# Kernel tuning notes

Measured on AMD Instinct MI355X. Metric: run time of the kernel, lower is better.

The kernel has to match this reference:

```python
import jax, jax.numpy as jnp
import numpy as np

B, L, H, V = 16, 1024, 512, 32000
HALF = H // 2
ALPHA = 0.95
EPS_NORM = 1e-12
EPS_LN = 1e-5


def setup_inputs() -> dict:
    key = jax.random.key(0)
    ks = jax.random.split(key, 12)
    s = 0.02
    return {
        "seq": jax.random.randint(ks[0], (B, L), 0, V),
        "embed": jax.random.normal(ks[1], (V, H), jnp.float32) * s,
        "ff_w1": jax.random.normal(ks[2], (2 * H, H), jnp.float32) * s,
        "ff_b1": jnp.zeros((2 * H,), jnp.float32),
        "ff_w2": jax.random.normal(ks[3], (H, 2 * H), jnp.float32) * s,
        "ff_b2": jnp.zeros((H,), jnp.float32),
        "gamma": jnp.ones((H,), jnp.float32),
        "beta": jnp.zeros((H,), jnp.float32),
        "sem_w": jax.random.normal(ks[4], (HALF, H), jnp.float32) * s,
        "epi_w": jax.random.normal(ks[5], (HALF, H), jnp.float32) * s,
        "rp_w": jax.random.normal(ks[6], (H, H), jnp.float32) * s,
        "rp_b": jnp.zeros((H,), jnp.float32),
        "out_w": jax.random.normal(ks[7], (V, H), jnp.float32) * s,
        "out_b": jnp.zeros((V,), jnp.float32),
    }


def _layernorm(x, gamma, beta):
    mu = jnp.mean(x, axis=-1, keepdims=True)
    var = jnp.mean(jnp.square(x - mu), axis=-1, keepdims=True)
    return (x - mu) * jax.lax.rsqrt(var + EPS_LN) * gamma + beta


def _l2norm(k):
    # F.normalize: k / max(||k||_2, eps)
    n = jnp.sqrt(jnp.sum(jnp.square(k), axis=-1, keepdims=True))
    return k / jnp.maximum(n, EPS_NORM)


def reference(seq, embed, ff_w1, ff_b1, ff_w2, ff_b2, gamma, beta,
              sem_w, epi_w, rp_w, rp_b, out_w, out_b):
    h = embed[seq]  # [B, L, H]
    ff = jnp.maximum(jnp.einsum('blh,fh->blf', h, ff_w1) + ff_b1, 0.0)
    ff = jnp.einsum('blf,hf->blh', ff, ff_w2) + ff_b2
    h = _layernorm(h + ff, gamma, beta)  # [B, L, H]

    # precompute all keys, time-major for scan: [L, B, half]
    ks_all = jnp.einsum('blh,ch->lbc', h, sem_w)
    ke_all = jnp.einsum('blh,ch->lbc', h, epi_w)

    def step(carry, inp):
        Ms, Me = carry                      # [B, half, half]
        ks, ke = inp                        # [B, half]
        kns = _l2norm(ks)
        kne = _l2norm(ke)
        vps = jnp.einsum('bij,bj->bi', Ms, kns)
        vpe = jnp.einsum('bij,bj->bi', Me, kne)
        Ds = (ks - vps)[:, :, None] * kns[:, None, :]
        De = (ke - vpe)[:, :, None] * kne[:, None, :]
        Ms = Ms + (1.0 - ALPHA) * Ds
        Me = Me + (1.0 - ALPHA) * De
        return (Ms, Me), None

    M0 = jnp.zeros((B, HALF, HALF), h.dtype)
    (M_s, M_e), _ = jax.lax.scan(step, (M0, M0), (ks_all[:L - 1], ke_all[:L - 1]))

    qs = ks_all[L - 1]  # sem_p(h[:, -1])
    qe = ke_all[L - 1]  # epi_p(h[:, -1])
    cs = jnp.einsum('bij,bj->bi', M_s, qs)
    ce = jnp.einsum('bij,bj->bi', M_e, qe)
    c = jnp.concatenate([cs, ce], axis=-1)  # [B, H]
    r = jnp.einsum('bh,gh->bg', c, rp_w) + rp_b
    return jnp.einsum('bh,vh->bv', r, out_w) + out_b  # [B, V]
```

## Files before the change

kernel.cpp:

```cpp
#include <hip/hip_runtime.h>
#include <stdint.h>

#define Bsz 16
#define Lsz 1024
#define Hsz 512
#define Vsz 32000
#define HALF 256
#define BETA 0.05f

typedef unsigned short u16;
typedef __attribute__((ext_vector_type(8))) short short8;
typedef __attribute__((ext_vector_type(4))) float f32x4;

__device__ __forceinline__ float bf2f(u16 u) { return __uint_as_float(((unsigned int)u) << 16); }
__device__ __forceinline__ u16 f2bf(float f) {
    unsigned int u = __float_as_uint(f);
    return (u16)((u + 0x7FFFu + ((u >> 16) & 1u)) >> 16);
}
__device__ __forceinline__ u16 f2h(float f) {
    _Float16 h = (_Float16)f;
    return *(u16*)&h;
}
__device__ __forceinline__ bool mode_f32(const void* gamma) {
    return *(const unsigned int*)gamma == 0x3F800000u;
}

__device__ __forceinline__ float wave_sum(float p) {
    p += __shfl_xor(p, 32, 64);
    p += __shfl_xor(p, 16, 64);
    p += __shfl_xor(p, 8, 64);
    p += __shfl_xor(p, 4, 64);
    p += __shfl_xor(p, 2, 64);
    p += __shfl_xor(p, 1, 64);
    return p;
}

__device__ __forceinline__ void cvt8(const void* src, u16* dst, int i, bool f32m) {
    union { u16 u[8]; uint4 q; } o;
    if (f32m) {
        const float* s = (const float*)src + i;
        const float4 a = *(const float4*)s;
        const float4 b = *(const float4*)(s + 4);
        o.u[0] = f2bf(a.x); o.u[1] = f2bf(a.y); o.u[2] = f2bf(a.z); o.u[3] = f2bf(a.w);
        o.u[4] = f2bf(b.x); o.u[5] = f2bf(b.y); o.u[6] = f2bf(b.z); o.u[7] = f2bf(b.w);
    } else {
        o.q = *(const uint4*)((const u16*)src + i);
    }
    *(uint4*)(dst + i) = o.q;
}

__global__ __launch_bounds__(256)
void cvt_all(const void* s0, const void* s1, const void* s2, const void* s3,
             const void* s4, const void* s5, const void* s6, const void* s7,
             const void* s8, const void* s9, const void* s10,
             u16* d0, u16* d1, u16* d2, u16* d3, u16* d4, u16* d5, u16* d6,
             u16* d7, u16* d8, u16* d9, u16* d10, const void* gamma) {
    const bool f32m = mode_f32(gamma);
    const int g = blockIdx.x * 256 + threadIdx.x;
    const void* src; u16* dst; int off;
    if      (g < 65536)  { src = s0;  dst = d0;  off = g; }
    else if (g < 131072) { src = s1;  dst = d1;  off = g - 65536; }
    else if (g < 147456) { src = s2;  dst = d2;  off = g - 131072; }
    else if (g < 163840) { src = s3;  dst = d3;  off = g - 147456; }
    else if (g < 196608) { src = s4;  dst = d4;  off = g - 163840; }
    else if (g < 196736) { src = s5;  dst = d5;  off = g - 196608; }
    else if (g < 196800) { src = s6;  dst = d6;  off = g - 196736; }
    else if (g < 196864) { src = s7;  dst = d7;  off = g - 196800; }
    else if (g < 196928) { src = s8;  dst = d8;  off = g - 196864; }
    else if (g < 196992) { src = s9;  dst = d9;  off = g - 196928; }
    else if (g < 200992) { src = s10; dst = d10; off = g - 196992; }
    else return;
    cvt8(src, dst, off * 8, f32m);
}

__global__ __launch_bounds__(256)
void gather_kernel(const int* __restrict__ seq, const void* __restrict__ embed,
                   u16* __restrict__ h0, const void* __restrict__ gamma) {
    const bool f32m = mode_f32(gamma);
    const int row = blockIdx.x * 4 + (threadIdx.x >> 6);
    const int lane = threadIdx.x & 63;
    const int tok = seq[row];
    union { u16 u[8]; uint4 q; } o;
    if (f32m) {
        const float* e = (const float*)embed + (size_t)tok * Hsz + lane * 8;
        const float4 a = *(const float4*)e;
        const float4 b = *(const float4*)(e + 4);
        o.u[0] = f2bf(a.x); o.u[1] = f2bf(a.y); o.u[2] = f2bf(a.z); o.u[3] = f2bf(a.w);
        o.u[4] = f2bf(b.x); o.u[5] = f2bf(b.y); o.u[6] = f2bf(b.z); o.u[7] = f2bf(b.w);
    } else {
        o.q = *((const uint4*)((const u16*)embed + (size_t)tok * Hsz) + lane);
    }
    *((uint4*)(h0 + (size_t)row * Hsz) + lane) = o.q;
}

template <int EPI>
__global__ __launch_bounds__(256)
void gemm128(const u16* __restrict__ A, const u16* __restrict__ B0,
             const u16* __restrict__ B1, const u16* __restrict__ bias,
             const u16* resid, void* Cout, u16* __restrict__ kT,
             int M, int N, int K) {
    __shared__ u16 Als[128 * 32];
    __shared__ u16 Bls[128 * 32];
    const int tid = threadIdx.x;
    const int wave = tid >> 6, lane = tid & 63;
    const int m0 = blockIdx.y * 128, n0 = blockIdx.x * 128;

    const u16* Bt;
    if (EPI == 2) Bt = (n0 < HALF) ? (B0 + (size_t)n0 * K) : (B1 + (size_t)(n0 - HALF) * K);
    else          Bt = B0 + (size_t)n0 * K;
    const u16* At = A + (size_t)m0 * K;

    const int wm = wave >> 1, wn = wave & 1;
    const int srow = lane >> 2;
    const int sk = (lane & 3) * 8;
    const int fr = lane & 15;
    const int fq = (lane >> 4) * 8;

    f32x4 acc[4][4];
#pragma unroll
    for (int i = 0; i < 4; i++)
#pragma unroll
        for (int j = 0; j < 4; j++) acc[i][j] = (f32x4){0.f, 0.f, 0.f, 0.f};

    for (int k0 = 0; k0 < K; k0 += 32) {
        __syncthreads();
#pragma unroll
        for (int c = 0; c < 2; c++) {
            const int ch = wave * 2 + c;
            const int row = ch * 16 + srow;
            __builtin_amdgcn_global_load_lds(
                (const __attribute__((address_space(1))) uint32_t*)(At + (size_t)row * K + k0 + sk),
                (__attribute__((address_space(3))) uint32_t*)(&Als[ch * 512]), 16, 0, 0);
            __builtin_amdgcn_global_load_lds(
                (const __attribute__((address_space(1))) uint32_t*)(Bt + (size_t)row * K + k0 + sk),
                (__attribute__((address_space(3))) uint32_t*)(&Bls[ch * 512]), 16, 0, 0);
        }
        __syncthreads();
        short8 af[4], bfr[4];
#pragma unroll
        for (int i = 0; i < 4; i++)
            af[i] = *(const short8*)&Als[(wm * 64 + i * 16 + fr) * 32 + fq];
#pragma unroll
        for (int j = 0; j < 4; j++)
            bfr[j] = *(const short8*)&Bls[(wn * 64 + j * 16 + fr) * 32 + fq];
#pragma unroll
        for (int i = 0; i < 4; i++)
#pragma unroll
            for (int j = 0; j < 4; j++)
                acc[i][j] = __builtin_amdgcn_mfma_f32_16x16x32_bf16(af[i], bfr[j], acc[i][j], 0, 0, 0);
    }

#pragma unroll
    for (int i = 0; i < 4; i++) {
#pragma unroll
        for (int j = 0; j < 4; j++) {
            const int n = n0 + wn * 64 + j * 16 + fr;
            if (EPI == 2) {
                const int mbase = m0 + wm * 64 + i * 16 + (lane >> 4) * 4;
                const int mem = n >> 8, col = n & 255;
                const int b = mbase >> 10, t0 = mbase & 1023;
                u16 tv[4];
#pragma unroll
                for (int r = 0; r < 4; r++) {
                    const int t = t0 + r;
                    const u16 bv = f2bf(acc[i][j][r]);
                    tv[r] = bv;
                    ((u16*)Cout)[((size_t)(mem * Bsz + b) * Lsz + t) * HALF + col] = bv;
                }
                const size_t kaddr = (size_t)(mem * Bsz + b) * 262144
                                   + (size_t)(t0 >> 6) * 16384
                                   + (size_t)((t0 >> 3) & 7) * 2048
                                   + (size_t)col * 8 + (t0 & 7);
                *(uint2*)&kT[kaddr] = *(uint2*)tv;
            } else {
#pragma unroll
                for (int r = 0; r < 4; r++) {
                    const int m = m0 + wm * 64 + i * 16 + (lane >> 4) * 4 + r;
                    float v = acc[i][j][r];
                    if (EPI == 0) {
                        v += bf2f(bias[n]);
                        v = v > 0.f ? v : 0.f;
                        ((u16*)Cout)[(size_t)m * N + n] = f2bf(v);
                    } else {
                        v += bf2f(bias[n]) + bf2f(resid[(size_t)m * N + n]);
                        ((u16*)Cout)[(size_t)m * N + n] = f2bf(v);
                    }
                }
            }
        }
    }
}

__global__ __launch_bounds__(256)
void ln_kernel(const u16* hs, const u16* __restrict__ gamma,
               const u16* __restrict__ beta, u16* hn) {
    const int row = blockIdx.x * 4 + (threadIdx.x >> 6);
    const int lane = threadIdx.x & 63;
    const uint4 raw = *(const uint4*)(hs + (size_t)row * Hsz + lane * 8);
    const u16* xr = (const u16*)&raw;
    float v[8];
#pragma unroll
    for (int j = 0; j < 8; j++) v[j] = bf2f(xr[j]);
    float s = 0.f;
#pragma unroll
    for (int j = 0; j < 8; j++) s += v[j];
    s = wave_sum(s);
    const float mu = s * (1.f / 512.f);
    float q = 0.f;
#pragma unroll
    for (int j = 0; j < 8; j++) { v[j] -= mu; q += v[j] * v[j]; }
    q = wave_sum(q);
    const float rstd = rsqrtf(q * (1.f / 512.f) + 1e-5f);
    union { u16 u[8]; uint4 qv; } o;
#pragma unroll
    for (int j = 0; j < 8; j++) {
        const int n = lane * 8 + j;
        o.u[j] = f2bf(v[j] * rstd * bf2f(gamma[n]) + bf2f(beta[n]));
    }
    *(uint4*)(hn + (size_t)row * Hsz + lane * 8) = o.qv;
}

__global__ __launch_bounds__(256)
void normalize_kernel(u16* kb, float* __restrict__ norms, float* __restrict__ invs) {
    const int row = blockIdx.x * 4 + (threadIdx.x >> 6);
    const int lane = threadIdx.x & 63;
    u16* p = kb + (size_t)row * HALF + lane * 4;
    uint2 raw = *(uint2*)p;
    const u16* kp = (const u16*)&raw;
    float f[4];
#pragma unroll
    for (int j = 0; j < 4; j++) f[j] = bf2f(kp[j]);
    float s = f[0]*f[0] + f[1]*f[1] + f[2]*f[2] + f[3]*f[3];
    s = wave_sum(s);
    const float n = fmaxf(sqrtf(s), 1e-12f);
    const float inv = 1.f / n;
    union { u16 u[4]; uint2 q; } o;
#pragma unroll
    for (int j = 0; j < 4; j++) o.u[j] = f2bf(f[j] * inv);
    *(uint2*)p = o.q;
    if (lane == 0) { norms[row] = n; invs[row] = inv; }
}

__global__ __launch_bounds__(256)
void gramsolve_kernel(const u16* __restrict__ kn, u16* __restrict__ W) {
    __shared__ u16 ls[64 * 264];
    __shared__ float Gl[64 * 64];
    const int mb = blockIdx.x, c = blockIdx.y;
    const int tid = threadIdx.x;
    const u16* src = kn + ((size_t)mb * Lsz + c * 64) * HALF;
    {
        const int row = tid >> 2, p = tid & 3;
        const u16* sp = src + row * 256 + p * 64;
        u16* dp = ls + row * 264 + p * 64;
#pragma unroll
        for (int i = 0; i < 8; i++)
            *(uint4*)(dp + i * 8) = *(const uint4*)(sp + i * 8);
    }
    __syncthreads();
    const int wave = tid >> 6, lane = tid & 63;
    const int fr = lane & 15, fq = (lane >> 4) * 8;
    f32x4 acc[4];
#pragma unroll
    for (int j = 0; j < 4; j++) acc[j] = (f32x4){0.f, 0.f, 0.f, 0.f};
    for (int k0 = 0; k0 < 256; k0 += 32) {
        const short8 a = *(const short8*)&ls[(wave * 16 + fr) * 264 + k0 + fq];
#pragma unroll
        for (int j = 0; j < 4; j++) {
            const short8 b = *(const short8*)&ls[(j * 16 + fr) * 264 + k0 + fq];
            acc[j] = __builtin_amdgcn_mfma_f32_16x16x32_bf16(a, b, acc[j], 0, 0, 0);
        }
    }
#pragma unroll
    for (int j = 0; j < 4; j++)
#pragma unroll
        for (int r = 0; r < 4; r++)
            Gl[(wave * 16 + (lane >> 4) * 4 + r) * 64 + j * 16 + fr] = acc[j][r];
    __syncthreads();

    const bool last = (c == 15);
    float w[64];
#pragma unroll
    for (int t = 63; t >= 0; --t) {
        float a0 = 0.f, a1 = 0.f, a2 = 0.f, a3 = 0.f;
        const int q0 = (t + 4) & ~3;
#pragma unroll
        for (int tp = t + 1; tp < q0; ++tp) a0 += Gl[t * 64 + tp] * w[tp];
#pragma unroll
        for (int q = q0; q < 64; q += 4) {
            const f32x4 g = *(const f32x4*)&Gl[t * 64 + q];
            a0 += g[0] * w[q];     a1 += g[1] * w[q + 1];
            a2 += g[2] * w[q + 2]; a3 += g[3] * w[q + 3];
        }
        float wt = bf2f(ls[t * 264 + tid]) - BETA * ((a0 + a1) + (a2 + a3));
        if (last && t == 63) wt = 0.f;
        w[t] = wt;
    }
    __syncthreads();
    {
        const int i_ = (tid >> 3) & 7, p_ = tid >> 6, e_ = tid & 7;
#pragma unroll
        for (int t = 0; t < 64; t++)
            ls[i_ * 2056 + (t * 4 + p_) * 8 + e_] = f2h(w[t]);
    }
    __syncthreads();
    u16* Wc = W + ((size_t)mb * 16 + c) * 16384;
#pragma unroll
    for (int i2 = 0; i2 < 8; i2++)
        *(uint4*)(Wc + i2 * 2048 + tid * 8) = *(const uint4*)(ls + i2 * 2056 + tid * 8);
}

__global__ __launch_bounds__(256, 1)
void scan3_kernel(const u16* __restrict__ kn, const u16* __restrict__ kT,
                  const float* __restrict__ norms, const float* __restrict__ invs,
                  const u16* __restrict__ W, float* __restrict__ cbuf) {
    __shared__ float uL[256], suL[64], scL[64];
    const int mb = blockIdx.x;
    const int tid = threadIdx.x;
    const int t = tid >> 2, p = tid & 3;
    const float* nb = norms + (size_t)mb * Lsz;
    const float* ib = invs + (size_t)mb * Lsz;

    float u = bf2f(kn[((size_t)mb * Lsz + 1023) * HALF + tid]) * nb[1023];
    float cacc = 0.f;
    uL[tid] = u;

    const u16* kTmb = kT + (size_t)mb * 262144;
    const u16* Wmb  = W  + (size_t)mb * 262144;

    uint4 wA[8], kA[8], wB[8], kB[8];
    {
        const u16* wp = Wmb + (size_t)15 * 16384;
        const u16* kp = kTmb + (size_t)15 * 16384;
#pragma unroll
        for (int i = 0; i < 8; i++) wA[i] = *(const uint4*)(wp + i * 2048 + tid * 8);
#pragma unroll
        for (int i = 0; i < 8; i++) kA[i] = *(const uint4*)(kp + i * 2048 + tid * 8);
    }
    asm volatile("s_waitcnt lgkmcnt(0)" ::: "memory");
    __builtin_amdgcn_s_barrier();

    auto process = [&](const uint4 (&WR)[8], const uint4 (&KQ)[8], const int c) {
        {
            float pa = 0.f, pb = 0.f;
#pragma unroll
            for (int i = 0; i < 8; i++) {
                union { uint4 q; _Float16 h[8]; } wv; wv.q = WR[i];
                const f32x4 u0 = *(const f32x4*)&uL[p * 64 + i * 8];
                const f32x4 u1 = *(const f32x4*)&uL[p * 64 + i * 8 + 4];
                pa += (float)wv.h[0] * u0[0] + (float)wv.h[1] * u0[1]
                    + (float)wv.h[2] * u0[2] + (float)wv.h[3] * u0[3];
                pb += (float)wv.h[4] * u1[0] + (float)wv.h[5] * u1[1]
                    + (float)wv.h[6] * u1[2] + (float)wv.h[7] * u1[3];
            }
            float part = pa + pb;
            part += __shfl_xor(part, 1, 64);
            part += __shfl_xor(part, 2, 64);
            if (p == 0) { suL[t] = part * ib[c * 64 + t]; scL[t] = part; }
        }
        asm volatile("s_waitcnt lgkmcnt(0)" ::: "memory");
        __builtin_amdgcn_s_barrier();
        {
            float du0 = 0.f, du1 = 0.f, dc0 = 0.f, dc1 = 0.f;
#pragma unroll
            for (int i = 0; i < 8; i++) {
                const u16* kk = (const u16*)&KQ[i];
                const f32x4 sa = *(const f32x4*)&suL[i * 8];
                const f32x4 sb = *(const f32x4*)&suL[i * 8 + 4];
                const f32x4 ca = *(const f32x4*)&scL[i * 8];
                const f32x4 cb = *(const f32x4*)&scL[i * 8 + 4];
                const float k0 = bf2f(kk[0]), k1 = bf2f(kk[1]);
                const float k2 = bf2f(kk[2]), k3 = bf2f(kk[3]);
                const float k4 = bf2f(kk[4]), k5 = bf2f(kk[5]);
                const float k6 = bf2f(kk[6]), k7 = bf2f(kk[7]);
                du0 += sa[0] * k0 + sa[1] * k1 + sa[2] * k2 + sa[3] * k3;
                du1 += sb[0] * k4 + sb[1] * k5 + sb[2] * k6 + sb[3] * k7;
                dc0 += ca[0] * k0 + ca[1] * k1 + ca[2] * k2 + ca[3] * k3;
                dc1 += cb[0] * k4 + cb[1] * k5 + cb[2] * k6 + cb[3] * k7;
            }
            u -= BETA * (du0 + du1);
            cacc += BETA * (dc0 + dc1);
            uL[tid] = u;
        }
        asm volatile("s_waitcnt lgkmcnt(0)" ::: "memory");
        __builtin_amdgcn_s_barrier();
    };

    for (int cc = 15; cc >= 1; cc -= 2) {
        {
            const u16* wp = Wmb + (size_t)(cc - 1) * 16384;
            const u16* kp = kTmb + (size_t)(cc - 1) * 16384;
#pragma unroll
            for (int i = 0; i < 8; i++) wB[i] = *(const uint4*)(wp + i * 2048 + tid * 8);
#pragma unroll
            for (int i = 0; i < 8; i++) kB[i] = *(const uint4*)(kp + i * 2048 + tid * 8);
        }
        __builtin_amdgcn_sched_barrier(0);
        process(wA, kA, cc);
        if (cc >= 3) {
            const u16* wp = Wmb + (size_t)(cc - 2) * 16384;
            const u16* kp = kTmb + (size_t)(cc - 2) * 16384;
#pragma unroll
            for (int i = 0; i < 8; i++) wA[i] = *(const uint4*)(wp + i * 2048 + tid * 8);
#pragma unroll
            for (int i = 0; i < 8; i++) kA[i] = *(const uint4*)(kp + i * 2048 + tid * 8);
        }
        __builtin_amdgcn_sched_barrier(0);
        process(wB, kB, cc - 1);
    }
    const int b = mb & 15, mem = mb >> 4;
    cbuf[(size_t)b * Hsz + mem * HALF + tid] = cacc;
}

__global__ __launch_bounds__(256)
void rproj_kernel(const float* __restrict__ cbuf, const u16* __restrict__ rpw,
                  const u16* __restrict__ rpb, u16* __restrict__ rbuf) {
    __shared__ float cl[Hsz];
    const int b = blockIdx.x, tid = threadIdx.x;
    cl[tid] = cbuf[(size_t)b * Hsz + tid];
    cl[tid + 256] = cbuf[(size_t)b * Hsz + 256 + tid];
    __syncthreads();
#pragma unroll
    for (int gg = 0; gg < 2; gg++) {
        const int g = gg * 256 + tid;
        const u16* wr = rpw + (size_t)g * Hsz;
        float acc = bf2f(rpb[g]);
        for (int k = 0; k < Hsz; k += 8) {
            const uint4 w8 = *(const uint4*)(wr + k);
            const u16* w = (const u16*)&w8;
            const float4 c0 = *(const float4*)&cl[k];
            const float4 c1 = *(const float4*)&cl[k + 4];
            acc += bf2f(w[0]) * c0.x + bf2f(w[1]) * c0.y + bf2f(w[2]) * c0.z + bf2f(w[3]) * c0.w
                 + bf2f(w[4]) * c1.x + bf2f(w[5]) * c1.y + bf2f(w[6]) * c1.z + bf2f(w[7]) * c1.w;
        }
        rbuf[(size_t)b * Hsz + g] = f2bf(acc);
    }
}

__global__ __launch_bounds__(256)
void logits_kernel(const u16* __restrict__ rbuf, const void* __restrict__ outw,
                   const u16* __restrict__ outb, void* __restrict__ out,
                   const void* __restrict__ gamma) {
    __shared__ u16 rls[16 * Hsz];
    const bool f32m = mode_f32(gamma);
    const int tid = threadIdx.x;
    {
        const uint4* src = (const uint4*)rbuf;
        uint4* dst = (uint4*)rls;
#pragma unroll
        for (int i = 0; i < 4; i++) dst[i * 256 + tid] = src[i * 256 + tid];
    }
    __syncthreads();
    const int wave = tid >> 6, lane = tid & 63;
    const int n0 = blockIdx.x * 256 + wave * 64;
    const int fr = lane & 15, fq = (lane >> 4) * 8;
    f32x4 acc[4];
#pragma unroll
    for (int j = 0; j < 4; j++) acc[j] = (f32x4){0.f, 0.f, 0.f, 0.f};
    if (f32m) {
        for (int k0 = 0; k0 < Hsz; k0 += 32) {
            const short8 af = *(const short8*)&rls[fr * Hsz + k0 + fq];
#pragma unroll
            for (int j = 0; j < 4; j++) {
                const float* wp = (const float*)outw + (size_t)(n0 + j * 16 + fr) * Hsz + k0 + fq;
                const float4 a = *(const float4*)wp;
                const float4 bq = *(const float4*)(wp + 4);
                union { u16 u[8]; short8 v; } bb;
                bb.u[0] = f2bf(a.x); bb.u[1] = f2bf(a.y); bb.u[2] = f2bf(a.z); bb.u[3] = f2bf(a.w);
                bb.u[4] = f2bf(bq.x); bb.u[5] = f2bf(bq.y); bb.u[6] = f2bf(bq.z); bb.u[7] = f2bf(bq.w);
                acc[j] = __builtin_amdgcn_mfma_f32_16x16x32_bf16(af, bb.v, acc[j], 0, 0, 0);
            }
        }
    } else {
        for (int k0 = 0; k0 < Hsz; k0 += 32) {
            const short8 af = *(const short8*)&rls[fr * Hsz + k0 + fq];
#pragma unroll
            for (int j = 0; j < 4; j++) {
                const short8 b8 = *(const short8*)((const u16*)outw + (size_t)(n0 + j * 16 + fr) * Hsz + k0 + fq);
                acc[j] = __builtin_amdgcn_mfma_f32_16x16x32_bf16(af, b8, acc[j], 0, 0, 0);
            }
        }
    }
#pragma unroll
    for (int j = 0; j < 4; j++) {
        const int v = n0 + j * 16 + fr;
        const float bv = bf2f(outb[v]);
#pragma unroll
        for (int r = 0; r < 4; r++) {
            const int bb = (lane >> 4) * 4 + r;
            const float val = acc[j][r] + bv;
            if (f32m) ((float*)out)[(size_t)bb * Vsz + v] = val;
            else      ((u16*)out)[(size_t)bb * Vsz + v] = f2bf(val);
        }
    }
}

extern "C" void kernel_launch(void* const* d_in, const int* in_sizes, int n_in,
                              void* d_out, int out_size, void* d_ws, size_t ws_size,
                              hipStream_t stream) {
    const int*  seq   = (const int*)d_in[0];
    const void* embed = d_in[1];
    const void* ffw1  = d_in[2];
    const void* ffb1  = d_in[3];
    const void* ffw2  = d_in[4];
    const void* ffb2  = d_in[5];
    const void* gamma = d_in[6];
    const void* beta  = d_in[7];
    const void* semw  = d_in[8];
    const void* epiw  = d_in[9];
    const void* rpw   = d_in[10];
    const void* rpb   = d_in[11];
    const void* outw  = d_in[12];
    const void* outb  = d_in[13];

    char* ws = (char*)d_ws;
    u16*   h0    = (u16*)(ws + 0);
    u16*   Wbuf  = (u16*)(ws + 0);
    u16*   C1    = (u16*)(ws + (size_t)0x1000000);
    u16*   kbuf  = (u16*)(ws + (size_t)0x1000000);
    u16*   kT    = (u16*)(ws + (size_t)0x2000000);
    size_t off   = 50331648;
    float* norms = (float*)(ws + off); off += (size_t)32 * Lsz * 4;
    float* invs  = (float*)(ws + off); off += (size_t)32 * Lsz * 4;
    u16* cffw1 = (u16*)(ws + off); off += (size_t)1024 * 512 * 2;
    u16* cffw2 = (u16*)(ws + off); off += (size_t)512 * 1024 * 2;
    u16* csemw = (u16*)(ws + off); off += (size_t)256 * 512 * 2;
    u16* cepiw = (u16*)(ws + off); off += (size_t)256 * 512 * 2;
    u16* crpw  = (u16*)(ws + off); off += (size_t)512 * 512 * 2;
    u16* cffb1 = (u16*)(ws + off); off += 1024 * 2;
    u16* cffb2 = (u16*)(ws + off); off += 512 * 2;
    u16* cgam  = (u16*)(ws + off); off += 512 * 2;
    u16* cbet  = (u16*)(ws + off); off += 512 * 2;
    u16* crpb  = (u16*)(ws + off); off += 512 * 2;
    u16* coutb = (u16*)(ws + off); off += (size_t)32000 * 2;
    off = (off + 255) & ~(size_t)255;
    float* cbuf = (float*)(ws + off); off += (size_t)16 * 512 * 4;
    u16*   rbuf = (u16*)(ws + off);

    cvt_all<<<786, 256, 0, stream>>>(ffw1, ffw2, semw, epiw, rpw, ffb1, ffb2,
                                     gamma, beta, rpb, outb,
                                     cffw1, cffw2, csemw, cepiw, crpw, cffb1, cffb2,
                                     cgam, cbet, crpb, coutb, gamma);
    gather_kernel<<<4096, 256, 0, stream>>>(seq, embed, h0, gamma);
    gemm128<0><<<dim3(8, 128), 256, 0, stream>>>(h0, cffw1, nullptr, cffb1, nullptr, C1,
                                                 nullptr, 16384, 1024, 512);
    gemm128<1><<<dim3(4, 128), 256, 0, stream>>>(C1, cffw2, nullptr, cffb2, h0, h0,
                                                 nullptr, 16384, 512, 1024);
    ln_kernel<<<4096, 256, 0, stream>>>(h0, cgam, cbet, h0);
    gemm128<2><<<dim3(4, 128), 256, 0, stream>>>(h0, csemw, cepiw, nullptr, nullptr, kbuf,
                                                 kT, 16384, 512, 512);
    normalize_kernel<<<8192, 256, 0, stream>>>(kbuf, norms, invs);
    gramsolve_kernel<<<dim3(32, 16), 256, 0, stream>>>(kbuf, Wbuf);
    scan3_kernel<<<32, 256, 0, stream>>>(kbuf, kT, norms, invs, Wbuf, cbuf);
    rproj_kernel<<<16, 256, 0, stream>>>(cbuf, crpw, crpb, rbuf);
    logits_kernel<<<125, 256, 0, stream>>>(rbuf, outw, coutb, d_out, gamma);
}
```

Measured before the change: 372.6 us.

## Move chunk triangular solve into scan; gram kernel emits Gram and transposed keys

Replaces the gramsolve kernel, which computed per-chunk W matrices by a 64-step triangular solve over all 256 columns, with a lighter gram kernel. That kernel only writes the fp16 Gram matrix and a transposed copy of the normalized keys. The scan kernel then solves for the 64 chunk coefficients per step in a single wave, using a readlane-based forward substitution over the Gram row. This removes most of the precompute work and the write and read of the W matrices. The cost is a 64-step serial dependency chain added to the already sequential scan, and the Gram buffer now overwrites the key buffer in place.

```diff
diff --git a/kernel.cpp b/kernel.cpp
--- a/kernel.cpp
+++ b/kernel.cpp
@@ -242,9 +242,9 @@
 }
 
 __global__ __launch_bounds__(256)
-void gramsolve_kernel(const u16* __restrict__ kn, u16* __restrict__ W) {
+void gram_kernel(const u16* __restrict__ kn, u16* __restrict__ Gt,
+                 u16* __restrict__ knT) {
     __shared__ u16 ls[64 * 264];
-    __shared__ float Gl[64 * 64];
     const int mb = blockIdx.x, c = blockIdx.y;
     const int tid = threadIdx.x;
     const u16* src = kn + ((size_t)mb * Lsz + c * 64) * HALF;
@@ -270,92 +270,101 @@
             acc[j] = __builtin_amdgcn_mfma_f32_16x16x32_bf16(a, b, acc[j], 0, 0, 0);
         }
     }
-#pragma unroll
-    for (int j = 0; j < 4; j++)
-#pragma unroll
-        for (int r = 0; r < 4; r++)
-            Gl[(wave * 16 + (lane >> 4) * 4 + r) * 64 + j * 16 + fr] = acc[j][r];
-    __syncthreads();
-
-    const bool last = (c == 15);
-    float w[64];
-#pragma unroll
-    for (int t = 63; t >= 0; --t) {
-        float a0 = 0.f, a1 = 0.f, a2 = 0.f, a3 = 0.f;
-        const int q0 = (t + 4) & ~3;
-#pragma unroll
-        for (int tp = t + 1; tp < q0; ++tp) a0 += Gl[t * 64 + tp] * w[tp];
-#pragma unroll
-        for (int q = q0; q < 64; q += 4) {
-            const f32x4 g = *(const f32x4*)&Gl[t * 64 + q];
-            a0 += g[0] * w[q];     a1 += g[1] * w[q + 1];
-            a2 += g[2] * w[q + 2]; a3 += g[3] * w[q + 3];
-        }
-        float wt = bf2f(ls[t * 264 + tid]) - BETA * ((a0 + a1) + (a2 + a3));
-        if (last && t == 63) wt = 0.f;
-        w[t] = wt;
-    }
-    __syncthreads();
-    {
-        const int i_ = (tid >> 3) & 7, p_ = tid >> 6, e_ = tid & 7;
-#pragma unroll
-        for (int t = 0; t < 64; t++)
-            ls[i_ * 2056 + (t * 4 + p_) * 8 + e_] = f2h(w[t]);
-    }
-    __syncthreads();
-    u16* Wc = W + ((size_t)mb * 16 + c) * 16384;
-#pragma unroll
-    for (int i2 = 0; i2 < 8; i2++)
-        *(uint4*)(Wc + i2 * 2048 + tid * 8) = *(const uint4*)(ls + i2 * 2056 + tid * 8);
+    u16* Gc = Gt + ((size_t)mb * 16 + c) * 16384;
+#pragma unroll
+    for (int j = 0; j < 4; j++) {
+        const int col = j * 16 + fr;
+#pragma unroll
+        for (int r = 0; r < 4; r++) {
+            const int row = wave * 16 + (lane >> 4) * 4 + r;
+            Gc[(col >> 3) * 512 + row * 8 + (col & 7)] = f2h(acc[j][r]);
+        }
+    }
+    u16* Tc = knT + ((size_t)mb * 16 + c) * 16384;
+#pragma unroll
+    for (int r2 = 0; r2 < 8; r2++) {
+        const int q = tid + 256 * r2;
+        const int i_ = q >> 8, l_ = q & 255;
+        *(uint4*)(Tc + (size_t)q * 8) =
+            *(const uint4*)(ls + (l_ >> 2) * 264 + (l_ & 3) * 64 + i_ * 8);
+    }
 }
 
 __global__ __launch_bounds__(256, 1)
-void scan3_kernel(const u16* __restrict__ kn, const u16* __restrict__ kT,
-                  const float* __restrict__ norms, const float* __restrict__ invs,
-                  const u16* __restrict__ W, float* __restrict__ cbuf) {
-    __shared__ float uL[256], suL[64], scL[64];
+void scan4_kernel(const u16* __restrict__ knT, const u16* __restrict__ kT,
+                  const u16* __restrict__ Gt, const float* __restrict__ norms,
+                  const float* __restrict__ invs, float* __restrict__ cbuf) {
+    __shared__ float uL[256], dL[64], suL[64], scL[64];
     const int mb = blockIdx.x;
     const int tid = threadIdx.x;
     const int t = tid >> 2, p = tid & 3;
-    const float* nb = norms + (size_t)mb * Lsz;
+    const int wave = tid >> 6, lane = tid & 63;
     const float* ib = invs + (size_t)mb * Lsz;
 
-    float u = bf2f(kn[((size_t)mb * Lsz + 1023) * HALF + tid]) * nb[1023];
+    const u16* knTmb = knT + (size_t)mb * 262144;
+    const u16* kTmb  = kT  + (size_t)mb * 262144;
+    const u16* Gmb   = Gt  + (size_t)mb * 262144;
+
+    float u = bf2f(knTmb[15 * 16384 + ((tid >> 3) & 7) * 2048
+                         + (252 + (tid >> 6)) * 8 + (tid & 7)])
+              * norms[(size_t)mb * Lsz + 1023];
     float cacc = 0.f;
     uL[tid] = u;
 
-    const u16* kTmb = kT + (size_t)mb * 262144;
-    const u16* Wmb  = W  + (size_t)mb * 262144;
-
-    uint4 wA[8], kA[8], wB[8], kB[8];
+    uint4 nA[8], kA[8], gA[8], nB[8], kB[8], gB[8];
     {
-        const u16* wp = Wmb + (size_t)15 * 16384;
-        const u16* kp = kTmb + (size_t)15 * 16384;
-#pragma unroll
-        for (int i = 0; i < 8; i++) wA[i] = *(const uint4*)(wp + i * 2048 + tid * 8);
+        const u16* np = knTmb + 15 * 16384;
+        const u16* kp = kTmb + 15 * 16384;
+#pragma unroll
+        for (int i = 0; i < 8; i++) nA[i] = *(const uint4*)(np + i * 2048 + tid * 8);
 #pragma unroll
         for (int i = 0; i < 8; i++) kA[i] = *(const uint4*)(kp + i * 2048 + tid * 8);
+        if (wave == 0) {
+            const u16* gp = Gmb + 15 * 16384;
+#pragma unroll
+            for (int i = 0; i < 8; i++) gA[i] = *(const uint4*)(gp + i * 512 + lane * 8);
+        }
     }
     asm volatile("s_waitcnt lgkmcnt(0)" ::: "memory");
     __builtin_amdgcn_s_barrier();
 
-    auto process = [&](const uint4 (&WR)[8], const uint4 (&KQ)[8], const int c) {
+    auto process = [&](const uint4 (&NR)[8], const uint4 (&KQ)[8],
+                       const uint4 (&GR)[8], const int c) {
         {
             float pa = 0.f, pb = 0.f;
 #pragma unroll
             for (int i = 0; i < 8; i++) {
-                union { uint4 q; _Float16 h[8]; } wv; wv.q = WR[i];
+                const u16* kk = (const u16*)&NR[i];
                 const f32x4 u0 = *(const f32x4*)&uL[p * 64 + i * 8];
                 const f32x4 u1 = *(const f32x4*)&uL[p * 64 + i * 8 + 4];
-                pa += (float)wv.h[0] * u0[0] + (float)wv.h[1] * u0[1]
-                    + (float)wv.h[2] * u0[2] + (float)wv.h[3] * u0[3];
-                pb += (float)wv.h[4] * u1[0] + (float)wv.h[5] * u1[1]
-                    + (float)wv.h[6] * u1[2] + (float)wv.h[7] * u1[3];
+                pa += bf2f(kk[0]) * u0[0] + bf2f(kk[1]) * u0[1]
+                    + bf2f(kk[2]) * u0[2] + bf2f(kk[3]) * u0[3];
+                pb += bf2f(kk[4]) * u1[0] + bf2f(kk[5]) * u1[1]
+                    + bf2f(kk[6]) * u1[2] + bf2f(kk[7]) * u1[3];
             }
             float part = pa + pb;
             part += __shfl_xor(part, 1, 64);
             part += __shfl_xor(part, 2, 64);
-            if (p == 0) { suL[t] = part * ib[c * 64 + t]; scL[t] = part; }
+            if (p == 0) dL[t] = part;
+        }
+        asm volatile("s_waitcnt lgkmcnt(0)" ::: "memory");
+        __builtin_amdgcn_s_barrier();
+        if (wave == 0) {
+            const float d = dL[lane];
+            const float myinv = ib[c * 64 + lane];
+            float r = 0.f, sv = 0.f;
+#pragma unroll
+            for (int tp = 63; tp >= 0; --tp) {
+                const float cand = d - BETA * r;
+                float s = __uint_as_float(
+                    __builtin_amdgcn_readlane(__float_as_uint(cand), tp));
+                if (c == 15 && tp == 63) s = 0.f;
+                if (lane == tp) sv = s;
+                const _Float16* gh = (const _Float16*)&GR[tp >> 3];
+                r += (float)gh[tp & 7] * s;
+            }
+            suL[lane] = sv * myinv;
+            scL[lane] = sv;
         }
         asm volatile("s_waitcnt lgkmcnt(0)" ::: "memory");
         __builtin_amdgcn_s_barrier();
@@ -387,25 +396,35 @@
 
     for (int cc = 15; cc >= 1; cc -= 2) {
         {
-            const u16* wp = Wmb + (size_t)(cc - 1) * 16384;
+            const u16* np = knTmb + (size_t)(cc - 1) * 16384;
             const u16* kp = kTmb + (size_t)(cc - 1) * 16384;
 #pragma unroll
-            for (int i = 0; i < 8; i++) wB[i] = *(const uint4*)(wp + i * 2048 + tid * 8);
+            for (int i = 0; i < 8; i++) nB[i] = *(const uint4*)(np + i * 2048 + tid * 8);
 #pragma unroll
             for (int i = 0; i < 8; i++) kB[i] = *(const uint4*)(kp + i * 2048 + tid * 8);
+            if (wave == 0) {
+                const u16* gp = Gmb + (size_t)(cc - 1) * 16384;
+#pragma unroll
+                for (int i = 0; i < 8; i++) gB[i] = *(const uint4*)(gp + i * 512 + lane * 8);
+            }
         }
         __builtin_amdgcn_sched_barrier(0);
-        process(wA, kA, cc);
+        process(nA, kA, gA, cc);
         if (cc >= 3) {
-            const u16* wp = Wmb + (size_t)(cc - 2) * 16384;
+            const u16* np = knTmb + (size_t)(cc - 2) * 16384;
             const u16* kp = kTmb + (size_t)(cc - 2) * 16384;
 #pragma unroll
-            for (int i = 0; i < 8; i++) wA[i] = *(const uint4*)(wp + i * 2048 + tid * 8);
+            for (int i = 0; i < 8; i++) nA[i] = *(const uint4*)(np + i * 2048 + tid * 8);
 #pragma unroll
             for (int i = 0; i < 8; i++) kA[i] = *(const uint4*)(kp + i * 2048 + tid * 8);
+            if (wave == 0) {
+                const u16* gp = Gmb + (size_t)(cc - 2) * 16384;
+#pragma unroll
+                for (int i = 0; i < 8; i++) gA[i] = *(const uint4*)(gp + i * 512 + lane * 8);
+            }
         }
         __builtin_amdgcn_sched_barrier(0);
-        process(wB, kB, cc - 1);
+        process(nB, kB, gB, cc - 1);
     }
     const int b = mb & 15, mem = mb >> 4;
     cbuf[(size_t)b * Hsz + mem * HALF + tid] = cacc;
@@ -514,7 +533,7 @@
 
     char* ws = (char*)d_ws;
     u16*   h0    = (u16*)(ws + 0);
-    u16*   Wbuf  = (u16*)(ws + 0);
+    u16*   knT   = (u16*)(ws + 0);
     u16*   C1    = (u16*)(ws + (size_t)0x1000000);
     u16*   kbuf  = (u16*)(ws + (size_t)0x1000000);
     u16*   kT    = (u16*)(ws + (size_t)0x2000000);
@@ -549,8 +568,8 @@
     gemm128<2><<<dim3(4, 128), 256, 0, stream>>>(h0, csemw, cepiw, nullptr, nullptr, kbuf,
                                                  kT, 16384, 512, 512);
     normalize_kernel<<<8192, 256, 0, stream>>>(kbuf, norms, invs);
-    gramsolve_kernel<<<dim3(32, 16), 256, 0, stream>>>(kbuf, Wbuf);
-    scan3_kernel<<<32, 256, 0, stream>>>(kbuf, kT, norms, invs, Wbuf, cbuf);
+    gram_kernel<<<dim3(32, 16), 256, 0, stream>>>(kbuf, kbuf, knT);
+    scan4_kernel<<<32, 256, 0, stream>>>(knT, kT, kbuf, norms, invs, cbuf);
     rproj_kernel<<<16, 256, 0, stream>>>(cbuf, crpw, crpb, rbuf);
     logits_kernel<<<125, 256, 0, stream>>>(rbuf, outw, coutb, d_out, gamma);
 }
```

Result: no change. 380.0 us (+2.0%).
